# Optimization experiments

Hardware: AMD Instinct MI355X
Metric: run time of the kernel (lower is better)

The kernel has to match this reference:

```python
import jax, jax.numpy as jnp
import numpy as np

H = 128
N = 20000
E = 640000

def _lin_params(key, fan_in, fan_out, bias=True):
    k1, k2 = jax.random.split(key)
    bound = 1.0 / np.sqrt(fan_in)
    W = jax.random.uniform(k1, (fan_in, fan_out), jnp.float32, -bound, bound)
    if bias:
        b = jax.random.uniform(k2, (fan_out,), jnp.float32, -bound, bound)
        return W, b
    return W, None

def setup_inputs() -> dict:
    key = jax.random.key(0)
    ks = jax.random.split(key, 10)
    h = jax.random.normal(ks[0], (N, H), jnp.float32)
    pos = jax.random.normal(ks[1], (N, 3), jnp.float32)
    edge_index = jax.random.randint(ks[2], (2, E), 0, N, jnp.int64)
    eW1, eb1 = _lin_params(ks[3], 2 * H + 1, H)
    eW2, eb2 = _lin_params(ks[4], H, H)
    cW1, cb1 = _lin_params(ks[5], H, H)
    cW2, _ = _lin_params(ks[6], H, 1, bias=False)
    nW1, nb1 = _lin_params(ks[7], 2 * H, H)
    nW2, nb2 = _lin_params(ks[8], H, H)
    return {"h": h, "pos": pos, "edge_index": edge_index,
            "eW1": eW1, "eb1": eb1, "eW2": eW2, "eb2": eb2,
            "cW1": cW1, "cb1": cb1, "cW2": cW2,
            "nW1": nW1, "nb1": nb1, "nW2": nW2, "nb2": nb2}

def reference(h, pos, edge_index, eW1, eb1, eW2, eb2, cW1, cb1, cW2, nW1, nb1, nW2, nb2):
    row, col = edge_index[0], edge_index[1]
    n = h.shape[0]
    # per-edge geometry
    coord_diff = pos[row] - pos[col]                      # [E, 3]
    sq_dists = jnp.sum(coord_diff ** 2, axis=-1, keepdims=True)  # [E, 1]
    # edge MLP: Linear -> SiLU -> Linear -> SiLU
    edge_inputs = jnp.concatenate([h[row], h[col], sq_dists], axis=-1)  # [E, 2H+1]
    m_ij = jax.nn.silu(jax.nn.silu(edge_inputs @ eW1 + eb1) @ eW2 + eb2)  # [E, H]
    # coord MLP: Linear -> SiLU -> Linear(no bias) -> scalar weight per edge
    coord_weights = jax.nn.silu(m_ij @ cW1 + cb1) @ cW2   # [E, 1]
    norm_coord_diff = coord_diff / jnp.sqrt(sq_dists + 1e-8)
    pos_updates_ij = norm_coord_diff * coord_weights      # [E, 3]
    # scatter-mean over target nodes (zero where a node has no edges)
    pos_sum = jax.ops.segment_sum(pos_updates_ij, row, num_segments=n)
    cnt = jax.ops.segment_sum(jnp.ones((row.shape[0], 1), h.dtype), row, num_segments=n)
    pos_out = pos + pos_sum / jnp.maximum(cnt, 1.0)
    # scatter-add messages, then node MLP with residual
    m_i = jax.ops.segment_sum(m_ij, row, num_segments=n)  # [N, H]
    node_inputs = jnp.concatenate([h, m_i], axis=-1)      # [N, 2H]
    h_out = h + (jax.nn.silu(node_inputs @ nW1 + nb1) @ nW2 + nb2)
    return h_out, pos_out
```

## Files before the change

### kernel.cpp

```cpp
#include <hip/hip_runtime.h>
#include <hip/hip_bf16.h>
#include <cstdint>

#define H 128
#define NNODES 20000
#define NEDGES 640000
#define TILE 64
#define SCAN_BLOCKS 20
#define PQ_BLOCKS 313

typedef unsigned short ushort_t;
typedef __attribute__((ext_vector_type(8))) short short8;
typedef __attribute__((ext_vector_type(4))) float floatx4;
typedef __attribute__((ext_vector_type(2))) float floatx2;

__device__ __forceinline__ ushort_t f2bf(float f){
  uint32_t u = __builtin_bit_cast(uint32_t, f);
  u += 0x7fffu + ((u >> 16) & 1u);
  return (ushort_t)(u >> 16);
}
__device__ __forceinline__ uint32_t pk2bf(float lo, float hi){
  __hip_bfloat162 h2 = __float22bfloat162_rn(make_float2(lo, hi));
  uint32_t u;
  __builtin_memcpy(&u, &h2, 4);
  return u;
}
__device__ __forceinline__ floatx2 bfpair2(uint32_t u){
  floatx2 r;
  r.x = __builtin_bit_cast(float, u << 16);
  r.y = __builtin_bit_cast(float, u & 0xffff0000u);
  return r;
}
__device__ __forceinline__ float silu_f(float x){
  float e = __builtin_amdgcn_exp2f(-1.44269504089f * x);
  return x * __builtin_amdgcn_rcpf(1.f + e);
}

__global__ void setup_kernel(const float* __restrict__ eW1, const float* __restrict__ eW2,
                             const float* __restrict__ cW1, const float* __restrict__ nW1,
                             const float* __restrict__ nW2, const int* __restrict__ ei,
                             ushort_t* __restrict__ eW1t, ushort_t* __restrict__ eW2t,
                             ushort_t* __restrict__ cW1t, ushort_t* __restrict__ nW1t,
                             ushort_t* __restrict__ nW2t, uint32_t* __restrict__ w256b,
                             int* __restrict__ hist){
  int idx = blockIdx.x * 256 + threadIdx.x;
  if (idx < 32768){
    int n = idx >> 8, k = idx & 255;
    eW1t[idx] = f2bf(eW1[k * H + n]);
  } else if (idx < 49152){
    int j = idx - 32768; int n = j >> 7, k = j & 127;
    eW2t[j] = f2bf(eW2[k * H + n]);
  } else if (idx < 65536){
    int j = idx - 49152; int n = j >> 7, k = j & 127;
    cW1t[j] = f2bf(cW1[k * H + n]);
  } else if (idx < 98304){
    int j = idx - 65536; int n = j >> 8, k = j & 255;
    nW1t[j] = f2bf(nW1[k * H + n]);
  } else if (idx < 114688){
    int j = idx - 98304; int n = j >> 7, k = j & 127;
    nW2t[j] = f2bf(nW2[k * H + n]);
  } else if (idx < 114752){
    int j = idx - 114688;
    w256b[j] = pk2bf(eW1[256 * H + 2*j], eW1[256 * H + 2*j + 1]);
  } else if (idx < 754752){
    int j = idx - 114752;
    atomicAdd(&hist[ei[j]], 1);
  }
}

__global__ void scan_kernel(const int* __restrict__ hist, int* __restrict__ head,
                            int* __restrict__ flags, int* __restrict__ excl){
  __shared__ int s[1024];
  __shared__ int prev_s;
  const int b = blockIdx.x, t = threadIdx.x;
  const int idx = b * 1024 + t;
  int v = (idx < NNODES) ? hist[idx] : 0;
  s[t] = v;
  __syncthreads();
  for (int off = 1; off < 1024; off <<= 1){
    int tmp = (t >= off) ? s[t - off] : 0;
    __syncthreads();
    s[t] += tmp;
    __syncthreads();
  }
  if (t == 0){
    int prev = 0;
    if (b > 0){
      while (atomicAdd(&flags[b], 0) == 0){}
      __threadfence();
      prev = atomicAdd(&excl[b], 0);
    }
    prev_s = prev;
    if (b < SCAN_BLOCKS - 1){
      atomicExch(&excl[b + 1], prev + s[1023]);
      __threadfence();
      atomicExch(&flags[b + 1], 1);
    }
  }
  __syncthreads();
  if (idx < NNODES) head[idx] = s[t] - v + prev_s;
}

__global__ void pqscatter_kernel(const float* __restrict__ h,
                                 const ushort_t* __restrict__ eW1t,
                                 const ushort_t* __restrict__ nW1t,
                                 const float* __restrict__ eb1,
                                 ushort_t* __restrict__ Pb, ushort_t* __restrict__ Qb,
                                 ushort_t* __restrict__ Rb,
                                 const int* __restrict__ ei, int* __restrict__ head,
                                 int2* __restrict__ spair){
  if (blockIdx.x >= PQ_BLOCKS){
    int idx = (blockIdx.x - PQ_BLOCKS) * 256 + threadIdx.x;
    if (idx < NEDGES){
      int r = ei[idx], c = ei[NEDGES + idx];
      int p = atomicAdd(&head[r], 1);
      spair[p] = make_int2(r, c);
    }
    return;
  }
  const int t = threadIdx.x;
  const int lane = t & 63, q = lane >> 4, ln = lane & 15;
  const int nb = (t >> 6) * 32;
  const int c0 = nb + 2 * ln;
  const int base = blockIdx.x * 64;

  floatx4 accP[4][2], accQ[4][2], accR[4][2];
  #pragma unroll
  for (int mt = 0; mt < 4; mt++)
    #pragma unroll
    for (int nt = 0; nt < 2; nt++){
      accP[mt][nt] = (floatx4)0.f; accQ[mt][nt] = (floatx4)0.f; accR[mt][nt] = (floatx4)0.f;
    }

  #pragma unroll
  for (int ks = 0; ks < 4; ks++){
    short8 a[4];
    #pragma unroll
    for (int mt = 0; mt < 4; mt++){
      int node = base + mt*16 + ln;
      if (node >= NNODES) node = NNODES - 1;
      const float* hp = h + (size_t)node * H + ks*32 + q*8;
      float4 v0 = *(const float4*)hp;
      float4 v1 = *(const float4*)(hp + 4);
      uint32_t tw[4];
      tw[0] = pk2bf(v0.x, v0.y); tw[1] = pk2bf(v0.z, v0.w);
      tw[2] = pk2bf(v1.x, v1.y); tw[3] = pk2bf(v1.z, v1.w);
      __builtin_memcpy(&a[mt], tw, 16);
    }
    short8 bP[2], bQ[2], bR[2];
    #pragma unroll
    for (int nt = 0; nt < 2; nt++){
      bP[nt] = *(const short8*)(eW1t + (size_t)(c0 + nt) * 256 + ks*32 + q*8);
      bQ[nt] = *(const short8*)(eW1t + (size_t)(c0 + nt) * 256 + 128 + ks*32 + q*8);
      bR[nt] = *(const short8*)(nW1t + (size_t)(c0 + nt) * 256 + ks*32 + q*8);
    }
    #pragma unroll
    for (int mt = 0; mt < 4; mt++)
      #pragma unroll
      for (int nt = 0; nt < 2; nt++){
        accP[mt][nt] = __builtin_amdgcn_mfma_f32_16x16x32_bf16(a[mt], bP[nt], accP[mt][nt], 0, 0, 0);
        accQ[mt][nt] = __builtin_amdgcn_mfma_f32_16x16x32_bf16(a[mt], bQ[nt], accQ[mt][nt], 0, 0, 0);
        accR[mt][nt] = __builtin_amdgcn_mfma_f32_16x16x32_bf16(a[mt], bR[nt], accR[mt][nt], 0, 0, 0);
      }
  }
  float2 e1 = *(const float2*)(eb1 + c0);
  #pragma unroll
  for (int mt = 0; mt < 4; mt++)
    #pragma unroll
    for (int r = 0; r < 4; r++){
      int node = base + mt*16 + q*4 + r;
      if (node < NNODES){
        *(uint32_t*)(Pb + (size_t)node * H + c0) = pk2bf(accP[mt][0][r] + e1.x, accP[mt][1][r] + e1.y);
        *(uint32_t*)(Qb + (size_t)node * H + c0) = pk2bf(accQ[mt][0][r], accQ[mt][1][r]);
        *(uint32_t*)(Rb + (size_t)node * H + c0) = pk2bf(accR[mt][0][r], accR[mt][1][r]);
      }
    }
}

__global__ __launch_bounds__(256, 8) void edge_kernel(
    const ushort_t* __restrict__ Pb, const ushort_t* __restrict__ Qb,
    const float* __restrict__ pos, const int2* __restrict__ spair,
    const uint32_t* __restrict__ w256b,
    const float* __restrict__ eb2, const float* __restrict__ cb1,
    const float* __restrict__ cW2,
    const ushort_t* __restrict__ eW2t, const ushort_t* __restrict__ cW1t,
    float* __restrict__ m_i, float* __restrict__ pos_sum)
{
  __shared__ __align__(16) ushort_t buf[TILE * 136];
  __shared__ int   row_l[TILE];
  __shared__ float sq_l[TILE];
  __shared__ float dx_l[TILE], dy_l[TILE], dz_l[TILE], w_l[TILE];

  const int t = threadIdx.x;
  const int base = blockIdx.x * TILE;
  const int lane = t & 63, q = lane >> 4, ln = lane & 15;
  const int nb = (t >> 6) * 32;
  const int c0 = nb + 2 * ln;

  {
    const int i = t >> 2, p = t & 3;
    int2 rc = spair[base + i];
    float ax = pos[rc.x*3+0] - pos[rc.y*3+0];
    float ay = pos[rc.x*3+1] - pos[rc.y*3+1];
    float az = pos[rc.x*3+2] - pos[rc.y*3+2];
    float sq = ax*ax + ay*ay + az*az;
    if (p == 0){
      row_l[i] = rc.x; sq_l[i] = sq;
      dx_l[i] = ax; dy_l[i] = ay; dz_l[i] = az;
      w_l[i] = 0.f;
    }
    floatx2 sq2; sq2.x = sq; sq2.y = sq;
    const uint4* Pp = (const uint4*)(Pb + (size_t)rc.x * H + p*32);
    const uint4* Qp = (const uint4*)(Qb + (size_t)rc.y * H + p*32);
    const uint4* Wp = (const uint4*)(w256b + p*16);
    ushort_t* dst = buf + i * 136 + p*32;
    #pragma unroll
    for (int j = 0; j < 4; j++){
      uint4 pv = Pp[j], qv = Qp[j], wv = Wp[j];
      uint32_t pvv[4] = {pv.x, pv.y, pv.z, pv.w};
      uint32_t qvv[4] = {qv.x, qv.y, qv.z, qv.w};
      uint32_t wvv[4] = {wv.x, wv.y, wv.z, wv.w};
      uint32_t outv[4];
      #pragma unroll
      for (int e = 0; e < 4; e++){
        floatx2 f = bfpair2(pvv[e]) + bfpair2(qvv[e]) + sq2 * bfpair2(wvv[e]);
        outv[e] = pk2bf(silu_f(f.x), silu_f(f.y));
      }
      uint4 out; __builtin_memcpy(&out, outv, 16);
      *(uint4*)(dst + j*8) = out;
    }
  }
  __syncthreads();

  floatx4 acc[4][2];

  #pragma unroll
  for (int mt = 0; mt < 4; mt++)
    #pragma unroll
    for (int nt = 0; nt < 2; nt++) acc[mt][nt] = (floatx4)0.f;
  #pragma unroll
  for (int ks = 0; ks < 4; ks++){
    short8 a[4], b[2];
    #pragma unroll
    for (int mt = 0; mt < 4; mt++)
      a[mt] = *(const short8*)(buf + (mt*16 + ln) * 136 + ks*32 + q*8);
    #pragma unroll
    for (int nt = 0; nt < 2; nt++)
      b[nt] = *(const short8*)(eW2t + (size_t)(c0 + nt) * 128 + ks*32 + q*8);
    #pragma unroll
    for (int mt = 0; mt < 4; mt++)
      #pragma unroll
      for (int nt = 0; nt < 2; nt++)
        acc[mt][nt] = __builtin_amdgcn_mfma_f32_16x16x32_bf16(a[mt], b[nt], acc[mt][nt], 0, 0, 0);
  }
  __syncthreads();
  {
    float2 e2 = *(const float2*)(eb2 + c0);
    #pragma unroll
    for (int mt = 0; mt < 4; mt++)
      #pragma unroll
      for (int r = 0; r < 4; r++){
        int m = mt*16 + q*4 + r;
        float f0 = silu_f(acc[mt][0][r] + e2.x);
        float f1 = silu_f(acc[mt][1][r] + e2.y);
        *(uint32_t*)(buf + m * 136 + c0) = pk2bf(f0, f1);
      }
  }
  __syncthreads();

  #pragma unroll
  for (int mt = 0; mt < 4; mt++)
    #pragma unroll
    for (int nt = 0; nt < 2; nt++) acc[mt][nt] = (floatx4)0.f;
  #pragma unroll
  for (int ks = 0; ks < 4; ks++){
    short8 a[4], b[2];
    #pragma unroll
    for (int mt = 0; mt < 4; mt++)
      a[mt] = *(const short8*)(buf + (mt*16 + ln) * 136 + ks*32 + q*8);
    #pragma unroll
    for (int nt = 0; nt < 2; nt++)
      b[nt] = *(const short8*)(cW1t + (size_t)(c0 + nt) * 128 + ks*32 + q*8);
    #pragma unroll
    for (int mt = 0; mt < 4; mt++)
      #pragma unroll
      for (int nt = 0; nt < 2; nt++)
        acc[mt][nt] = __builtin_amdgcn_mfma_f32_16x16x32_bf16(a[mt], b[nt], acc[mt][nt], 0, 0, 0);
  }
  {
    float2 c1 = *(const float2*)(cb1 + c0);
    float2 c2 = *(const float2*)(cW2 + c0);
    #pragma unroll
    for (int mt = 0; mt < 4; mt++)
      #pragma unroll
      for (int r = 0; r < 4; r++){
        float p = silu_f(acc[mt][0][r] + c1.x) * c2.x
                + silu_f(acc[mt][1][r] + c1.y) * c2.y;
        p += __shfl_xor(p, 1);
        p += __shfl_xor(p, 2);
        p += __shfl_xor(p, 4);
        p += __shfl_xor(p, 8);
        if (ln == 0) atomicAdd(&w_l[mt*16 + q*4 + r], p);
      }
  }
  __syncthreads();

  if (t < 128){
    int cp = (t & 63) * 2;
    int ms = (t >> 6) * 32;
    float a0 = 0.f, a1 = 0.f;
    int cur = row_l[ms];
    #pragma unroll 4
    for (int mm = 0; mm < 32; mm++){
      int m = ms + mm;
      int rr = row_l[m];
      uint32_t v = *(const uint32_t*)(buf + m * 136 + cp);
      if (rr != cur){
        unsafeAtomicAdd(&m_i[(size_t)cur * H + cp],     a0);
        unsafeAtomicAdd(&m_i[(size_t)cur * H + cp + 1], a1);
        a0 = 0.f; a1 = 0.f; cur = rr;
      }
      floatx2 f = bfpair2(v);
      a0 += f.x; a1 += f.y;
    }
    unsafeAtomicAdd(&m_i[(size_t)cur * H + cp],     a0);
    unsafeAtomicAdd(&m_i[(size_t)cur * H + cp + 1], a1);
  } else if (t < 131){
    const int d = t - 128;
    const float* src = (d == 0) ? dx_l : (d == 1) ? dy_l : dz_l;
    float accv = 0.f;
    int cur = row_l[0];
    for (int m = 0; m < TILE; m++){
      int rr = row_l[m];
      if (rr != cur){
        unsafeAtomicAdd(&pos_sum[cur*3 + d], accv);
        accv = 0.f; cur = rr;
      }
      float s = __builtin_amdgcn_rsqf(sq_l[m] + 1e-8f) * w_l[m];
      accv += src[m] * s;
    }
    unsafeAtomicAdd(&pos_sum[cur*3 + d], accv);
  }
}

__global__ __launch_bounds__(256, 8) void node_kernel(
    const float* __restrict__ h, const float* __restrict__ pos,
    const float* __restrict__ nb1, const float* __restrict__ nb2,
    const ushort_t* __restrict__ nW1t, const ushort_t* __restrict__ nW2t,
    const ushort_t* __restrict__ Rb,
    const float* __restrict__ m_i, const float* __restrict__ pos_sum,
    const int* __restrict__ hist,
    float* __restrict__ h_out, float* __restrict__ pos_out)
{
  __shared__ __align__(16) ushort_t bufT[32 * 136];
  const int t = threadIdx.x;
  const int base = blockIdx.x * 32;
  const int lane = t & 63, q = lane >> 4, ln = lane & 15;
  const int nb_ = (t >> 6) * 32;
  const int c0 = nb_ + 2 * ln;

  if (t < 32){
    int node = base + t;
    float c = fmaxf((float)hist[node], 1.f);
    float invc = __builtin_amdgcn_rcpf(c);
    pos_out[node*3+0] = pos[node*3+0] + pos_sum[node*3+0] * invc;
    pos_out[node*3+1] = pos[node*3+1] + pos_sum[node*3+1] * invc;
    pos_out[node*3+2] = pos[node*3+2] + pos_sum[node*3+2] * invc;
  }

  floatx4 acc[2][2];
  #pragma unroll
  for (int mt = 0; mt < 2; mt++)
    #pragma unroll
    for (int nt = 0; nt < 2; nt++) acc[mt][nt] = (floatx4)0.f;
  #pragma unroll
  for (int ks = 0; ks < 4; ks++){
    short8 a[2], b[2];
    #pragma unroll
    for (int mt = 0; mt < 2; mt++){
      const float* mp = m_i + (size_t)(base + mt*16 + ln) * H + ks*32 + q*8;
      float4 v0 = *(const float4*)mp;
      float4 v1 = *(const float4*)(mp + 4);
      uint32_t tw[4];
      tw[0] = pk2bf(v0.x, v0.y); tw[1] = pk2bf(v0.z, v0.w);
      tw[2] = pk2bf(v1.x, v1.y); tw[3] = pk2bf(v1.z, v1.w);
      __builtin_memcpy(&a[mt], tw, 16);
    }
    #pragma unroll
    for (int nt = 0; nt < 2; nt++)
      b[nt] = *(const short8*)(nW1t + (size_t)(c0 + nt) * 256 + 128 + ks*32 + q*8);
    #pragma unroll
    for (int mt = 0; mt < 2; mt++)
      #pragma unroll
      for (int nt = 0; nt < 2; nt++)
        acc[mt][nt] = __builtin_amdgcn_mfma_f32_16x16x32_bf16(a[mt], b[nt], acc[mt][nt], 0, 0, 0);
  }
  {
    float2 b1 = *(const float2*)(nb1 + c0);
    #pragma unroll
    for (int mt = 0; mt < 2; mt++)
      #pragma unroll
      for (int r = 0; r < 4; r++){
        int m = mt*16 + q*4 + r;
        int node = base + m;
        floatx2 rf = bfpair2(*(const uint32_t*)(Rb + (size_t)node * H + c0));
        float f0 = silu_f(acc[mt][0][r] + rf.x + b1.x);
        float f1 = silu_f(acc[mt][1][r] + rf.y + b1.y);
        *(uint32_t*)(bufT + m * 136 + c0) = pk2bf(f0, f1);
      }
  }
  __syncthreads();

  #pragma unroll
  for (int mt = 0; mt < 2; mt++)
    #pragma unroll
    for (int nt = 0; nt < 2; nt++) acc[mt][nt] = (floatx4)0.f;
  #pragma unroll
  for (int ks = 0; ks < 4; ks++){
    short8 a[2], b[2];
    #pragma unroll
    for (int mt = 0; mt < 2; mt++)
      a[mt] = *(const short8*)(bufT + (mt*16 + ln) * 136 + ks*32 + q*8);
    #pragma unroll
    for (int nt = 0; nt < 2; nt++)
      b[nt] = *(const short8*)(nW2t + (size_t)(c0 + nt) * 128 + ks*32 + q*8);
    #pragma unroll
    for (int mt = 0; mt < 2; mt++)
      #pragma unroll
      for (int nt = 0; nt < 2; nt++)
        acc[mt][nt] = __builtin_amdgcn_mfma_f32_16x16x32_bf16(a[mt], b[nt], acc[mt][nt], 0, 0, 0);
  }
  {
    float2 b2 = *(const float2*)(nb2 + c0);
    #pragma unroll
    for (int mt = 0; mt < 2; mt++)
      #pragma unroll
      for (int r = 0; r < 4; r++){
        int node = base + mt*16 + q*4 + r;
        const float2 hv = *(const float2*)(h + (size_t)node * H + c0);
        float2 o;
        o.x = hv.x + acc[mt][0][r] + b2.x;
        o.y = hv.y + acc[mt][1][r] + b2.y;
        *(float2*)(h_out + (size_t)node * H + c0) = o;
      }
  }
}

extern "C" void kernel_launch(void* const* d_in, const int* in_sizes, int n_in,
                              void* d_out, int out_size, void* d_ws, size_t ws_size,
                              hipStream_t stream){
  const float* h   = (const float*)d_in[0];
  const float* pos = (const float*)d_in[1];
  const int*   ei  = (const int*)d_in[2];
  const float* eW1 = (const float*)d_in[3];
  const float* eb1 = (const float*)d_in[4];
  const float* eW2 = (const float*)d_in[5];
  const float* eb2 = (const float*)d_in[6];
  const float* cW1 = (const float*)d_in[7];
  const float* cb1 = (const float*)d_in[8];
  const float* cW2 = (const float*)d_in[9];
  const float* nW1 = (const float*)d_in[10];
  const float* nb1 = (const float*)d_in[11];
  const float* nW2 = (const float*)d_in[12];
  const float* nb2 = (const float*)d_in[13];

  char* ws = (char*)d_ws;
  float*    m_i     = (float*)   (ws);
  float*    pos_sum = (float*)   (ws + 10240000);
  int*      hist    = (int*)     (ws + 10480000);
  int*      flags   = (int*)     (ws + 10560000);
  int*      excl    = (int*)     (ws + 10560128);
  int*      head    = (int*)     (ws + 10560256);
  int2*     spair   = (int2*)    (ws + 10644096);
  ushort_t* Pb      = (ushort_t*)(ws + 15764096);
  ushort_t* eW1t    = (ushort_t*)(ws + 20884096);
  ushort_t* eW2t    = (ushort_t*)(ws + 20949632);
  ushort_t* cW1t    = (ushort_t*)(ws + 20982400);
  ushort_t* nW1t    = (ushort_t*)(ws + 21015168);
  ushort_t* nW2t    = (ushort_t*)(ws + 21080704);
  ushort_t* Qb      = (ushort_t*)(ws + 21113472);
  ushort_t* Rb      = (ushort_t*)(ws + 26233472);
  uint32_t* w256b   = (uint32_t*)(ws + 31353472);

  (void)hipMemsetAsync(ws, 0, 10560256, stream);

  setup_kernel<<<2949, 256, 0, stream>>>(eW1, eW2, cW1, nW1, nW2, ei,
                                         eW1t, eW2t, cW1t, nW1t, nW2t, w256b, hist);
  scan_kernel<<<SCAN_BLOCKS, 1024, 0, stream>>>(hist, head, flags, excl);
  pqscatter_kernel<<<PQ_BLOCKS + (NEDGES + 255) / 256, 256, 0, stream>>>(
      h, eW1t, nW1t, eb1, Pb, Qb, Rb, ei, head, spair);

  edge_kernel<<<NEDGES / TILE, 256, 0, stream>>>(Pb, Qb, pos, spair, w256b,
                                                 eb2, cb1, cW2,
                                                 eW2t, cW1t, m_i, pos_sum);

  float* h_out   = (float*)d_out;
  float* pos_out = h_out + (size_t)NNODES * H;
  node_kernel<<<NNODES / 32, 256, 0, stream>>>(h, pos, nb1, nb2,
                                               nW1t, nW2t, Rb, m_i, pos_sum,
                                               hist, h_out, pos_out);
}
```

Baseline: 367.5 us.

## Fuse setup, scan and PQ/scatter into one persistent kernel with grid barriers

Replaces the setup, scan and pqscatter kernels and most of the workspace memset with a single persistent kernel of 256 blocks. Its phases are separated by atomic-counter grid barriers, and it zeroes the m_i and pos_sum buffers itself. This removes kernel launch gaps and the large memset, and uses a two-pass block scan instead of a serially chained one. In exchange, the PQ matmuls now run as three separate passes that reload h, and correctness depends on all 256 blocks being co-resident for the spin barriers.

Measured after the change: 391.9 us. 6.6% more time.

```diff
diff --git a/kernel.cpp b/kernel.cpp
--- a/kernel.cpp
+++ b/kernel.cpp
@@ -6,8 +6,8 @@
 #define NNODES 20000
 #define NEDGES 640000
 #define TILE 64
-#define SCAN_BLOCKS 20
 #define PQ_BLOCKS 313
+#define A_BLOCKS 256
 
 typedef unsigned short ushort_t;
 typedef __attribute__((ext_vector_type(8))) short short8;
@@ -36,102 +36,25 @@
   return x * __builtin_amdgcn_rcpf(1.f + e);
 }
 
-__global__ void setup_kernel(const float* __restrict__ eW1, const float* __restrict__ eW2,
-                             const float* __restrict__ cW1, const float* __restrict__ nW1,
-                             const float* __restrict__ nW2, const int* __restrict__ ei,
-                             ushort_t* __restrict__ eW1t, ushort_t* __restrict__ eW2t,
-                             ushort_t* __restrict__ cW1t, ushort_t* __restrict__ nW1t,
-                             ushort_t* __restrict__ nW2t, uint32_t* __restrict__ w256b,
-                             int* __restrict__ hist){
-  int idx = blockIdx.x * 256 + threadIdx.x;
-  if (idx < 32768){
-    int n = idx >> 8, k = idx & 255;
-    eW1t[idx] = f2bf(eW1[k * H + n]);
-  } else if (idx < 49152){
-    int j = idx - 32768; int n = j >> 7, k = j & 127;
-    eW2t[j] = f2bf(eW2[k * H + n]);
-  } else if (idx < 65536){
-    int j = idx - 49152; int n = j >> 7, k = j & 127;
-    cW1t[j] = f2bf(cW1[k * H + n]);
-  } else if (idx < 98304){
-    int j = idx - 65536; int n = j >> 8, k = j & 255;
-    nW1t[j] = f2bf(nW1[k * H + n]);
-  } else if (idx < 114688){
-    int j = idx - 98304; int n = j >> 7, k = j & 127;
-    nW2t[j] = f2bf(nW2[k * H + n]);
-  } else if (idx < 114752){
-    int j = idx - 114688;
-    w256b[j] = pk2bf(eW1[256 * H + 2*j], eW1[256 * H + 2*j + 1]);
-  } else if (idx < 754752){
-    int j = idx - 114752;
-    atomicAdd(&hist[ei[j]], 1);
-  }
-}
-
-__global__ void scan_kernel(const int* __restrict__ hist, int* __restrict__ head,
-                            int* __restrict__ flags, int* __restrict__ excl){
-  __shared__ int s[1024];
-  __shared__ int prev_s;
-  const int b = blockIdx.x, t = threadIdx.x;
-  const int idx = b * 1024 + t;
-  int v = (idx < NNODES) ? hist[idx] : 0;
-  s[t] = v;
-  __syncthreads();
-  for (int off = 1; off < 1024; off <<= 1){
-    int tmp = (t >= off) ? s[t - off] : 0;
-    __syncthreads();
-    s[t] += tmp;
-    __syncthreads();
-  }
-  if (t == 0){
-    int prev = 0;
-    if (b > 0){
-      while (atomicAdd(&flags[b], 0) == 0){}
-      __threadfence();
-      prev = atomicAdd(&excl[b], 0);
-    }
-    prev_s = prev;
-    if (b < SCAN_BLOCKS - 1){
-      atomicExch(&excl[b + 1], prev + s[1023]);
-      __threadfence();
-      atomicExch(&flags[b + 1], 1);
-    }
-  }
-  __syncthreads();
-  if (idx < NNODES) head[idx] = s[t] - v + prev_s;
-}
-
-__global__ void pqscatter_kernel(const float* __restrict__ h,
-                                 const ushort_t* __restrict__ eW1t,
-                                 const ushort_t* __restrict__ nW1t,
-                                 const float* __restrict__ eb1,
-                                 ushort_t* __restrict__ Pb, ushort_t* __restrict__ Qb,
-                                 ushort_t* __restrict__ Rb,
-                                 const int* __restrict__ ei, int* __restrict__ head,
-                                 int2* __restrict__ spair){
-  if (blockIdx.x >= PQ_BLOCKS){
-    int idx = (blockIdx.x - PQ_BLOCKS) * 256 + threadIdx.x;
-    if (idx < NEDGES){
-      int r = ei[idx], c = ei[NEDGES + idx];
-      int p = atomicAdd(&head[r], 1);
-      spair[p] = make_int2(r, c);
-    }
-    return;
-  }
-  const int t = threadIdx.x;
-  const int lane = t & 63, q = lane >> 4, ln = lane & 15;
-  const int nb = (t >> 6) * 32;
-  const int c0 = nb + 2 * ln;
-  const int base = blockIdx.x * 64;
-
-  floatx4 accP[4][2], accQ[4][2], accR[4][2];
+__device__ __forceinline__ void gsyncA(int* c){
+  __syncthreads();
+  if (threadIdx.x == 0){
+    __threadfence();
+    atomicAdd(c, 1);
+    while (atomicAdd(c, 0) < A_BLOCKS) {}
+    __threadfence();
+  }
+  __syncthreads();
+}
+
+__device__ __forceinline__ void pq_sub(const float* __restrict__ h,
+    const ushort_t* __restrict__ Wt, int koff, const float* __restrict__ bias,
+    ushort_t* __restrict__ Out, int base, int ln, int q, int c0){
+  floatx4 acc[4][2];
   #pragma unroll
   for (int mt = 0; mt < 4; mt++)
     #pragma unroll
-    for (int nt = 0; nt < 2; nt++){
-      accP[mt][nt] = (floatx4)0.f; accQ[mt][nt] = (floatx4)0.f; accR[mt][nt] = (floatx4)0.f;
-    }
-
+    for (int nt = 0; nt < 2; nt++) acc[mt][nt] = (floatx4)0.f;
   #pragma unroll
   for (int ks = 0; ks < 4; ks++){
     short8 a[4];
@@ -147,34 +70,141 @@
       tw[2] = pk2bf(v1.x, v1.y); tw[3] = pk2bf(v1.z, v1.w);
       __builtin_memcpy(&a[mt], tw, 16);
     }
-    short8 bP[2], bQ[2], bR[2];
-    #pragma unroll
-    for (int nt = 0; nt < 2; nt++){
-      bP[nt] = *(const short8*)(eW1t + (size_t)(c0 + nt) * 256 + ks*32 + q*8);
-      bQ[nt] = *(const short8*)(eW1t + (size_t)(c0 + nt) * 256 + 128 + ks*32 + q*8);
-      bR[nt] = *(const short8*)(nW1t + (size_t)(c0 + nt) * 256 + ks*32 + q*8);
-    }
-    #pragma unroll
-    for (int mt = 0; mt < 4; mt++)
-      #pragma unroll
-      for (int nt = 0; nt < 2; nt++){
-        accP[mt][nt] = __builtin_amdgcn_mfma_f32_16x16x32_bf16(a[mt], bP[nt], accP[mt][nt], 0, 0, 0);
-        accQ[mt][nt] = __builtin_amdgcn_mfma_f32_16x16x32_bf16(a[mt], bQ[nt], accQ[mt][nt], 0, 0, 0);
-        accR[mt][nt] = __builtin_amdgcn_mfma_f32_16x16x32_bf16(a[mt], bR[nt], accR[mt][nt], 0, 0, 0);
-      }
-  }
-  float2 e1 = *(const float2*)(eb1 + c0);
+    short8 bb[2];
+    #pragma unroll
+    for (int nt = 0; nt < 2; nt++)
+      bb[nt] = *(const short8*)(Wt + (size_t)(c0 + nt) * 256 + koff + ks*32 + q*8);
+    #pragma unroll
+    for (int mt = 0; mt < 4; mt++)
+      #pragma unroll
+      for (int nt = 0; nt < 2; nt++)
+        acc[mt][nt] = __builtin_amdgcn_mfma_f32_16x16x32_bf16(a[mt], bb[nt], acc[mt][nt], 0, 0, 0);
+  }
+  float2 e = make_float2(0.f, 0.f);
+  if (bias) e = *(const float2*)(bias + c0);
   #pragma unroll
   for (int mt = 0; mt < 4; mt++)
     #pragma unroll
     for (int r = 0; r < 4; r++){
       int node = base + mt*16 + q*4 + r;
-      if (node < NNODES){
-        *(uint32_t*)(Pb + (size_t)node * H + c0) = pk2bf(accP[mt][0][r] + e1.x, accP[mt][1][r] + e1.y);
-        *(uint32_t*)(Qb + (size_t)node * H + c0) = pk2bf(accQ[mt][0][r], accQ[mt][1][r]);
-        *(uint32_t*)(Rb + (size_t)node * H + c0) = pk2bf(accR[mt][0][r], accR[mt][1][r]);
-      }
-    }
+      if (node < NNODES)
+        *(uint32_t*)(Out + (size_t)node * H + c0) = pk2bf(acc[mt][0][r] + e.x, acc[mt][1][r] + e.y);
+    }
+}
+
+__global__ __launch_bounds__(256) void fusedA_kernel(
+    const float* __restrict__ h, const int* __restrict__ ei,
+    const float* __restrict__ eW1, const float* __restrict__ eb1,
+    const float* __restrict__ eW2, const float* __restrict__ cW1,
+    const float* __restrict__ nW1, const float* __restrict__ nW2,
+    char* __restrict__ ws)
+{
+  float4*   zbase  = (float4*)ws;
+  int*      hist   = (int*)(ws + 10480000);
+  int*      ctrs   = (int*)(ws + 10560000);
+  int*      totals = (int*)(ws + 10560064);
+  int*      head   = (int*)(ws + 10560256);
+  int2*     spair  = (int2*)(ws + 10644096);
+  ushort_t* Pb     = (ushort_t*)(ws + 15764096);
+  ushort_t* eW1t   = (ushort_t*)(ws + 20884096);
+  ushort_t* eW2t   = (ushort_t*)(ws + 20949632);
+  ushort_t* cW1t   = (ushort_t*)(ws + 20982400);
+  ushort_t* nW1t   = (ushort_t*)(ws + 21015168);
+  ushort_t* nW2t   = (ushort_t*)(ws + 21080704);
+  ushort_t* Qb     = (ushort_t*)(ws + 21113472);
+  ushort_t* Rb     = (ushort_t*)(ws + 26233472);
+  uint32_t* w256b  = (uint32_t*)(ws + 31353472);
+
+  __shared__ int sL[256];
+  __shared__ int off_s;
+
+  const int t = threadIdx.x, b = blockIdx.x;
+  const int gsz = A_BLOCKS * 256;
+
+  for (int idx = b*256 + t; idx < 1409752; idx += gsz){
+    if (idx < 32768){
+      int n = idx >> 8, k = idx & 255;
+      eW1t[idx] = f2bf(eW1[k * H + n]);
+    } else if (idx < 49152){
+      int j = idx - 32768; int n = j >> 7, k = j & 127;
+      eW2t[j] = f2bf(eW2[k * H + n]);
+    } else if (idx < 65536){
+      int j = idx - 49152; int n = j >> 7, k = j & 127;
+      cW1t[j] = f2bf(cW1[k * H + n]);
+    } else if (idx < 98304){
+      int j = idx - 65536; int n = j >> 8, k = j & 255;
+      nW1t[j] = f2bf(nW1[k * H + n]);
+    } else if (idx < 114688){
+      int j = idx - 98304; int n = j >> 7, k = j & 127;
+      nW2t[j] = f2bf(nW2[k * H + n]);
+    } else if (idx < 114752){
+      int j = idx - 114688;
+      w256b[j] = pk2bf(eW1[256 * H + 2*j], eW1[256 * H + 2*j + 1]);
+    } else if (idx < 754752){
+      int j = idx - 114752;
+      atomicAdd(&hist[ei[j]], 1);
+    } else {
+      int j = idx - 754752;
+      zbase[j] = make_float4(0.f, 0.f, 0.f, 0.f);
+    }
+  }
+  gsyncA(&ctrs[0]);
+
+  if (b < 20){
+    int base = b*1024 + t*4;
+    int v0 = (base+0 < NNODES) ? hist[base+0] : 0;
+    int v1 = (base+1 < NNODES) ? hist[base+1] : 0;
+    int v2 = (base+2 < NNODES) ? hist[base+2] : 0;
+    int v3 = (base+3 < NNODES) ? hist[base+3] : 0;
+    int tot = v0 + v1 + v2 + v3;
+    sL[t] = tot;
+    __syncthreads();
+    for (int off = 1; off < 256; off <<= 1){
+      int tmp = (t >= off) ? sL[t - off] : 0;
+      __syncthreads();
+      sL[t] += tmp;
+      __syncthreads();
+    }
+    int run = sL[t] - tot;
+    if (base+0 < NNODES) head[base+0] = run; run += v0;
+    if (base+1 < NNODES) head[base+1] = run; run += v1;
+    if (base+2 < NNODES) head[base+2] = run; run += v2;
+    if (base+3 < NNODES) head[base+3] = run;
+    if (t == 255) atomicExch(&totals[b], sL[255]);
+  }
+  gsyncA(&ctrs[1]);
+
+  if (b < 20){
+    if (t == 0){
+      int a = 0;
+      for (int i = 0; i < b; i++) a += atomicAdd(&totals[i], 0);
+      off_s = a;
+    }
+    __syncthreads();
+    int off = off_s;
+    for (int i = t; i < 1024; i += 256){
+      int idx = b*1024 + i;
+      if (idx < NNODES) head[idx] += off;
+    }
+  }
+  gsyncA(&ctrs[2]);
+
+  {
+    const int lane = t & 63, q = lane >> 4, ln = lane & 15;
+    const int nb = (t >> 6) * 32;
+    const int c0 = nb + 2 * ln;
+    for (int tile = b; tile < PQ_BLOCKS; tile += A_BLOCKS){
+      int base2 = tile * 64;
+      pq_sub(h, eW1t, 0,   eb1,     Pb, base2, ln, q, c0);
+      pq_sub(h, eW1t, 128, nullptr, Qb, base2, ln, q, c0);
+      pq_sub(h, nW1t, 0,   nullptr, Rb, base2, ln, q, c0);
+    }
+  }
+  for (int idx = b*256 + t; idx < NEDGES; idx += gsz){
+    int r = ei[idx], c = ei[NEDGES + idx];
+    int p = atomicAdd(&head[r], 1);
+    spair[p] = make_int2(r, c);
+  }
 }
 
 __global__ __launch_bounds__(256, 8) void edge_kernel(
@@ -468,12 +498,8 @@
   float*    m_i     = (float*)   (ws);
   float*    pos_sum = (float*)   (ws + 10240000);
   int*      hist    = (int*)     (ws + 10480000);
-  int*      flags   = (int*)     (ws + 10560000);
-  int*      excl    = (int*)     (ws + 10560128);
-  int*      head    = (int*)     (ws + 10560256);
   int2*     spair   = (int2*)    (ws + 10644096);
   ushort_t* Pb      = (ushort_t*)(ws + 15764096);
-  ushort_t* eW1t    = (ushort_t*)(ws + 20884096);
   ushort_t* eW2t    = (ushort_t*)(ws + 20949632);
   ushort_t* cW1t    = (ushort_t*)(ws + 20982400);
   ushort_t* nW1t    = (ushort_t*)(ws + 21015168);
@@ -482,13 +508,9 @@
   ushort_t* Rb      = (ushort_t*)(ws + 26233472);
   uint32_t* w256b   = (uint32_t*)(ws + 31353472);
 
-  (void)hipMemsetAsync(ws, 0, 10560256, stream);
-
-  setup_kernel<<<2949, 256, 0, stream>>>(eW1, eW2, cW1, nW1, nW2, ei,
-                                         eW1t, eW2t, cW1t, nW1t, nW2t, w256b, hist);
-  scan_kernel<<<SCAN_BLOCKS, 1024, 0, stream>>>(hist, head, flags, excl);
-  pqscatter_kernel<<<PQ_BLOCKS + (NEDGES + 255) / 256, 256, 0, stream>>>(
-      h, eW1t, nW1t, eb1, Pb, Qb, Rb, ei, head, spair);
+  (void)hipMemsetAsync(ws + 10480000, 0, 80064, stream);
+
+  fusedA_kernel<<<A_BLOCKS, 256, 0, stream>>>(h, ei, eW1, eb1, eW2, cW1, nW1, nW2, ws);
 
   edge_kernel<<<NEDGES / TILE, 256, 0, stream>>>(Pb, Qb, pos, spair, w256b,
                                                  eb2, cb1, cW2,
```
